# Kernel optimization log

Hardware: AMD Instinct MI355X
Metric: run time of the kernel (lower is better)

Reference implementation:

```python
import jax, jax.numpy as jnp
import numpy as np

# NOTE: SoftAttn (not shown in source) is assumed to be a channel-wise softmax over the
# kernel_size**2 attention maps, as is standard in involution/dynamic-conv designs.

def conv2d(x, w, b=None, stride=1, pad=0, dil=1):
    y = jax.lax.conv_general_dilated(
        x, w, (stride, stride), [(pad, pad), (pad, pad)],
        rhs_dilation=(dil, dil), dimension_numbers=('NCHW', 'OIHW', 'NCHW'))
    return y if b is None else y + b[None, :, None, None]

def prelu(x, a):
    return jnp.where(x >= 0, x, a * x)

def pixel_shuffle(x, r):
    b, c, h, w = x.shape
    x = x.reshape(b, c // (r * r), r, r, h, w)
    x = x.transpose(0, 1, 4, 2, 5, 3)  # b, c', h, r, w, r
    return x.reshape(b, c // (r * r), h * r, w * r)

def aflb(x, aw, ab, fw):
    # Adaptive Fine-grained Local Block: per-position attention over k^2 taps,
    # broadcast across input channels, then contracted with the conv weight.
    k = 3
    C = x.shape[1]
    att = jax.nn.softmax(conv2d(x, aw, ab, pad=1), axis=1)  # [b, k*k, H, W]
    # unfold (channel-major, spatial-minor, matching torch F.unfold)
    p = jax.lax.conv_general_dilated_patches(
        x, (k, k), (1, 1), [(1, 1), (1, 1)],
        dimension_numbers=('NCHW', 'OIHW', 'NCHW'))  # [b, C*k*k, H, W]
    b_, _, H, W = p.shape
    p = p.reshape(b_, C, k * k, H, W)
    atx = p * att[:, None]  # broadcast attention over channels
    return jnp.einsum('bcphw,ocp->bohw', atx, fw.reshape(fw.shape[0], C, k * k))

def rmrs(x, wa, ba, wb, bb, wc, bc, awA, abA, fwA, awB, abB, fwB):
    o = jnp.concatenate([
        conv2d(x, wa, ba, pad=1),
        conv2d(x, wb, bb, pad=2, dil=2),
        conv2d(x, wc, bc, pad=3, dil=3)], axis=1)
    o = aflb(o, awA, abA, fwA)
    o = aflb(o, awB, abB, fwB)
    return jax.nn.relu(o + x)


def setup_inputs() -> dict:
    key = jax.random.key(0)
    ks = iter(jax.random.split(key, 64))
    def rn(shape, s=0.05):
        return jax.random.normal(next(ks), shape, jnp.float32) * s
    a = lambda: jnp.full((1,), 0.25, jnp.float32)
    d = dict(
        ms_up=rn((2, 4, 256, 256), 1.0),
        ms_org=rn((2, 4, 64, 64), 1.0),
        pan=rn((2, 1, 256, 256), 1.0),
        w_up4=rn((64, 4, 3, 3)), b_up4=jnp.zeros(64, jnp.float32), a_up4=a(),
        w_blk53=rn((30, 5, 3, 3)), b_blk53=jnp.zeros(30, jnp.float32), a_blk53=a(),
        w_blk43=rn((30, 4, 3, 3)), b_blk43=jnp.zeros(30, jnp.float32), a_blk43=a(),
        w1a=rn((20, 60, 3, 3)), b1a=jnp.zeros(20, jnp.float32),
        w1b=rn((20, 60, 3, 3)), b1b=jnp.zeros(20, jnp.float32),
        w1c=rn((20, 60, 3, 3)), b1c=jnp.zeros(20, jnp.float32),
        aw1=rn((9, 60, 3, 3)), ab1=jnp.zeros(9, jnp.float32), fw1=rn((60, 60, 3, 3)),
        aw2=rn((9, 60, 3, 3)), ab2=jnp.zeros(9, jnp.float32), fw2=rn((60, 60, 3, 3)),
        w_blk2=rn((30, 60, 3, 3)), b_blk2=jnp.zeros(30, jnp.float32), a_blk2=a(),
        w2a=rn((10, 30, 3, 3)), b2a=jnp.zeros(10, jnp.float32),
        w2b=rn((10, 30, 3, 3)), b2b=jnp.zeros(10, jnp.float32),
        w2c=rn((10, 30, 3, 3)), b2c=jnp.zeros(10, jnp.float32),
        aw3=rn((9, 30, 3, 3)), ab3=jnp.zeros(9, jnp.float32), fw3=rn((30, 30, 3, 3)),
        aw4=rn((9, 30, 3, 3)), ab4=jnp.zeros(9, jnp.float32), fw4=rn((30, 30, 3, 3)),
        w_c6=rn((4, 30, 3, 3)), b_c6=jnp.zeros(4, jnp.float32),
    )
    return d


def reference(ms_up, ms_org, pan,
              w_up4, b_up4, a_up4,
              w_blk53, b_blk53, a_blk53,
              w_blk43, b_blk43, a_blk43,
              w1a, b1a, w1b, b1b, w1c, b1c,
              aw1, ab1, fw1, aw2, ab2, fw2,
              w_blk2, b_blk2, a_blk2,
              w2a, b2a, w2b, b2b, w2c, b2c,
              aw3, ab3, fw3, aw4, ab4, fw4,
              w_c6, b_c6):
    ms_org_up = prelu(pixel_shuffle(conv2d(ms_org, w_up4, b_up4, pad=1), 4), a_up4)
    data1 = jnp.concatenate([ms_org_up, pan], axis=1)  # [b,5,H,W]
    pan_conv = prelu(conv2d(data1, w_blk53, b_blk53, pad=1), a_blk53)
    ms_up_conv = prelu(conv2d(ms_up, w_blk43, b_blk43, pad=1), a_blk43)
    out1 = jnp.concatenate([ms_up_conv, pan_conv], axis=1)  # [b,60,H,W]
    out2 = rmrs(out1, w1a, b1a, w1b, b1b, w1c, b1c, aw1, ab1, fw1, aw2, ab2, fw2)
    out3 = prelu(conv2d(out2, w_blk2, b_blk2, pad=1), a_blk2)  # [b,30,H,W]
    out3 = rmrs(out3, w2a, b2a, w2b, b2b, w2c, b2c, aw3, ab3, fw3, aw4, ab4, fw4)
    out8 = conv2d(out3, w_c6, b_c6, pad=1)
    return out8 + ms_up
```

## Files before the change

kernel.cpp:

```cpp
#include <hip/hip_runtime.h>

typedef __attribute__((ext_vector_type(8))) short short8;
typedef __attribute__((ext_vector_type(4))) float f32x4;
typedef __attribute__((ext_vector_type(4))) int i32x4;

#define HW 65536

__device__ __forceinline__ float bf2f(unsigned short u){
    union { unsigned int i; float f; } x; x.i = ((unsigned int)u) << 16; return x.f;
}
__device__ __forceinline__ unsigned short f2bf(float f){
    union { float f; unsigned int i; } x; x.f = f;
    unsigned int r = x.i + 0x7fffu + ((x.i >> 16) & 1u);
    return (unsigned short)(r >> 16);
}
__device__ __forceinline__ unsigned int pack2(float a, float b){
    return (unsigned int)f2bf(a) | ((unsigned int)f2bf(b) << 16);
}
__device__ __forceinline__ i32x4 addrelu4(i32x4 a, i32x4 b){
    i32x4 o;
#pragma unroll
    for (int k = 0; k < 4; ++k) {
        unsigned int ua = (unsigned int)a[k], ub = (unsigned int)b[k];
        float x0 = bf2f((unsigned short)(ua & 0xffff)) + bf2f((unsigned short)(ub & 0xffff));
        float x1 = bf2f((unsigned short)(ua >> 16))    + bf2f((unsigned short)(ub >> 16));
        o[k] = (int)(((unsigned int)f2bf(fmaxf(x0, 0.f))) |
                     ((unsigned int)f2bf(fmaxf(x1, 0.f)) << 16));
    }
    return o;
}

template<int PRELU>
__global__ __launch_bounds__(256, 4) void sconv2_k(
    const unsigned short* __restrict__ inA, const unsigned short* __restrict__ wfA,
    const float* __restrict__ biasA, const float* __restrict__ alA, int coffA,
    const unsigned short* __restrict__ inB, const unsigned short* __restrict__ wfB,
    const float* __restrict__ biasB, const float* __restrict__ alB, int coffB,
    unsigned short* __restrict__ outb, int cpad)
{
    constexpr int KK = 1;
    constexpr int CPIN = 32, SGR = 4, SGRP = 5, SPX = 66;
    constexpr int NSTGDW = 3 * SPX * SGRP * 4;
    constexpr int ODP = 20;
    constexpr int OUTOFF = NSTGDW;
    __shared__ __align__(16) unsigned int sm[NSTGDW + 64 * ODP];
    const int tid = threadIdx.x;
    const int lane = tid & 63, wv = tid >> 6;
    const int col = lane & 15, g = lane >> 4;
    const int bx = blockIdx.x;
    const int xcd = bx & 7, t = bx >> 3;
    const int y0 = xcd * 32 + (t & 31);
    const int x0 = ((t >> 5) & 3) * 64;
    const int which = blockIdx.z >> 1, b = blockIdx.z & 1;
    const unsigned short* in = which ? inB : inA;
    const unsigned short* wfrag = which ? wfB : wfA;
    const float* bias = which ? biasB : biasA;
    const float* alphap = which ? alB : alA;
    const int coff = which ? coffB : coffA;
    const unsigned short* inb = in + (size_t)b * HW * CPIN;

#pragma unroll
    for (int rr = 0; rr < 3; ++rr) {
        const int yy = y0 + rr - 1;
        for (int u = tid; u < SPX * SGR; u += 256) {
            const int slot = u & (SGR - 1), px = u / SGR;
            const int xx = x0 - 1 + px;
            i32x4 v = {0,0,0,0};
            if ((unsigned)yy < 256u && (unsigned)xx < 256u)
                v = *(const i32x4*)(inb + (size_t)(yy * 256 + xx) * CPIN + slot * 8);
            *(i32x4*)&sm[((rr * SPX + px) * SGRP + slot) * 4] = v;
        }
    }
    if (tid < 64) sm[OUTOFF + tid * ODP + 15] = 0;
    __syncthreads();

    const short8* wp = (const short8*)wfrag;
    f32x4 acc[2][2];
#pragma unroll
    for (int mt = 0; mt < 2; ++mt)
#pragma unroll
        for (int c = 0; c < 2; ++c) acc[mt][c] = (f32x4){0.f,0.f,0.f,0.f};
#pragma unroll
    for (int tap = 0; tap < 9; ++tap) {
        const int dy = tap / 3 - 1, dx = tap % 3 - 1;
        const int rl = dy + 1;
        short8 af[2];
#pragma unroll
        for (int mt = 0; mt < 2; ++mt)
            af[mt] = wp[(tap * 2 + mt) * 64 + lane];
        const int pl = 1 + wv * 16 + col + dx;
        const int c2 = tap & 1;
        short8 bf = *(const short8*)&sm[((rl * SPX + pl) * SGRP + g) * 4];
#pragma unroll
        for (int mt = 0; mt < 2; ++mt)
            acc[mt][c2] = __builtin_amdgcn_mfma_f32_16x16x32_bf16(af[mt], bf, acc[mt][c2], 0, 0, 0);
    }
    const float al = PRELU ? __ldg(alphap) : 0.f;
    const int px = wv * 16 + col;
#pragma unroll
    for (int mt = 0; mt < 2; ++mt) {
        const f32x4 a = acc[mt][0] + acc[mt][1];
#pragma unroll
        for (int e = 0; e < 2; ++e) {
            const int rb = mt * 16 + g * 4 + e * 2;
            if (rb < 30) {
                float v0 = a[e * 2]     + __ldg(bias + rb);
                float v1 = a[e * 2 + 1] + ((rb + 1 < 30) ? __ldg(bias + rb + 1) : 0.f);
                if (PRELU) { v0 = v0 >= 0.f ? v0 : al * v0; v1 = v1 >= 0.f ? v1 : al * v1; }
                if (rb + 1 >= 30) v1 = 0.f;
                sm[OUTOFF + px * ODP + (rb >> 1)] = pack2(v0, v1);
            }
        }
    }
    __syncthreads();
    {
        const int slot = tid & 3, opx = tid >> 2;
        i32x4 v = *(i32x4*)&sm[OUTOFF + opx * ODP + slot * 4];
        const size_t go = ((size_t)b * HW + (size_t)y0 * 256 + x0 + opx) * cpad + coff + slot * 8;
        *(i32x4*)(outb + go) = v;
    }
}

template<int KK, int PRELU>
__global__ __launch_bounds__(256, 4) void sconv_k(
    const unsigned short* __restrict__ in,
    const unsigned short* __restrict__ wfrag,
    const float* __restrict__ bias,
    const float* __restrict__ alphap,
    unsigned short* __restrict__ outb, int cpad, int coff)
{
    constexpr int CPIN = KK * 32, SGR = KK * 4, SGRP = SGR + 1, SPX = 66;
    constexpr int NSTGDW = 3 * SPX * SGRP * 4;
    constexpr int ODP = 20;
    constexpr int OUTOFF = NSTGDW;
    __shared__ __align__(16) unsigned int sm[NSTGDW + 64 * ODP];
    const int tid = threadIdx.x;
    const int lane = tid & 63, wv = tid >> 6;
    const int col = lane & 15, g = lane >> 4;
    const int bx = blockIdx.x;
    const int xcd = bx & 7, t = bx >> 3;
    const int y0 = xcd * 32 + (t & 31);
    const int x0 = ((t >> 5) & 3) * 64;
    const int b = blockIdx.z;
    const unsigned short* inb = in + (size_t)b * HW * CPIN;

#pragma unroll
    for (int rr = 0; rr < 3; ++rr) {
        const int yy = y0 + rr - 1;
        for (int u = tid; u < SPX * SGR; u += 256) {
            const int slot = u & (SGR - 1), px = u / SGR;
            const int xx = x0 - 1 + px;
            i32x4 v = {0,0,0,0};
            if ((unsigned)yy < 256u && (unsigned)xx < 256u)
                v = *(const i32x4*)(inb + (size_t)(yy * 256 + xx) * CPIN + slot * 8);
            *(i32x4*)&sm[((rr * SPX + px) * SGRP + slot) * 4] = v;
        }
    }
    if (tid < 64) sm[OUTOFF + tid * ODP + 15] = 0;
    __syncthreads();

    const short8* wp = (const short8*)wfrag;
    f32x4 acc[2][2];
#pragma unroll
    for (int mt = 0; mt < 2; ++mt)
#pragma unroll
        for (int c = 0; c < 2; ++c) acc[mt][c] = (f32x4){0.f,0.f,0.f,0.f};
#pragma unroll
    for (int tap = 0; tap < 9; ++tap) {
        const int dy = tap / 3 - 1, dx = tap % 3 - 1;
        const int rl = dy + 1;
        short8 af[2][KK];
#pragma unroll
        for (int mt = 0; mt < 2; ++mt)
#pragma unroll
            for (int kk = 0; kk < KK; ++kk)
                af[mt][kk] = wp[((tap * 2 + mt) * KK + kk) * 64 + lane];
        const int pl = 1 + wv * 16 + col + dx;
#pragma unroll
        for (int kk = 0; kk < KK; ++kk) {
            const int c2 = (KK == 2) ? kk : (tap & 1);
            short8 bf = *(const short8*)&sm[((rl * SPX + pl) * SGRP + kk * 4 + g) * 4];
#pragma unroll
            for (int mt = 0; mt < 2; ++mt)
                acc[mt][c2] = __builtin_amdgcn_mfma_f32_16x16x32_bf16(af[mt][kk], bf, acc[mt][c2], 0, 0, 0);
        }
    }
    const float al = PRELU ? __ldg(alphap) : 0.f;
    const int px = wv * 16 + col;
#pragma unroll
    for (int mt = 0; mt < 2; ++mt) {
        const f32x4 a = acc[mt][0] + acc[mt][1];
#pragma unroll
        for (int e = 0; e < 2; ++e) {
            const int rb = mt * 16 + g * 4 + e * 2;
            if (rb < 30) {
                float v0 = a[e * 2]     + __ldg(bias + rb);
                float v1 = a[e * 2 + 1] + ((rb + 1 < 30) ? __ldg(bias + rb + 1) : 0.f);
                if (PRELU) { v0 = v0 >= 0.f ? v0 : al * v0; v1 = v1 >= 0.f ? v1 : al * v1; }
                if (rb + 1 >= 30) v1 = 0.f;
                sm[OUTOFF + px * ODP + (rb >> 1)] = pack2(v0, v1);
            }
        }
    }
    __syncthreads();
    {
        const int slot = tid & 3, opx = tid >> 2;
        i32x4 v = *(i32x4*)&sm[OUTOFF + opx * ODP + slot * 4];
        const size_t go = ((size_t)b * HW + (size_t)y0 * 256 + x0 + opx) * cpad + coff + slot * 8;
        *(i32x4*)(outb + go) = v;
    }
}

template<int KK, int MR>
__global__ __launch_bounds__(256, 4) void trident_s(
    const unsigned short* __restrict__ in,
    const unsigned short* __restrict__ wf0, const unsigned short* __restrict__ wf1,
    const unsigned short* __restrict__ wf2,
    const float* __restrict__ b0, const float* __restrict__ b1, const float* __restrict__ b2,
    unsigned short* __restrict__ outb)
{
    constexpr int CPIN = KK * 32, CPAD = KK * 32;
    constexpr int SGR = KK * 4, SGRP = SGR + 1, SPX = 70;
    constexpr int MT_ = (KK == 2) ? 2 : 1;
    constexpr int CPP = KK * 4, ODP = (CPP + 1) * 4;
    constexpr int NSTGDW = 3 * SPX * SGRP * 4;
    constexpr int OUTOFF = NSTGDW;
    constexpr int NG1 = SPX * SGR;
    constexpr int NIT2 = (2 * NG1 + 255) / 256;
    __shared__ __align__(16) unsigned int sm[NSTGDW + 64 * ODP];
    const int tid = threadIdx.x;
    const int lane = tid & 63, wv = tid >> 6;
    const int col = lane & 15, g = lane >> 4;
    const int bx = blockIdx.x;
    const int xcd = bx & 7, t = bx >> 3;
    const int y0 = xcd * 32 + (t & 31);
    const int x0 = ((t >> 5) & 3) * 64;
    const int b = blockIdx.z;
    const unsigned short* inb = in + (size_t)b * HW * CPIN;

    auto stage_row = [&](int srow, int yy) {
        for (int u = tid; u < NG1; u += 256) {
            const int slot = u & (SGR - 1), px = u / SGR;
            const int xx = x0 - 3 + px;
            i32x4 v = {0,0,0,0};
            if ((unsigned)yy < 256u && (unsigned)xx < 256u)
                v = *(const i32x4*)(inb + (size_t)(yy * 256 + xx) * CPIN + slot * 8);
            *(i32x4*)&sm[((srow * SPX + px) * SGRP + slot) * 4] = v;
        }
    };
    i32x4 Rp[NIT2], Rq[NIT2];
    auto issue_into = [&](int d, i32x4* R) {
#pragma unroll
        for (int it = 0; it < NIT2; ++it) {
            const int u = tid + it * 256;
            i32x4 v = {0,0,0,0};
            if (u < 2 * NG1) {
                const int r = (u >= NG1) ? 1 : 0;
                const int uu = u - r * NG1;
                const int slot = uu & (SGR - 1), px = uu / SGR;
                const int yy = y0 + (r ? d : -d);
                const int xx = x0 - 3 + px;
                if ((unsigned)yy < 256u && (unsigned)xx < 256u)
                    v = *(const i32x4*)(inb + (size_t)(yy * 256 + xx) * CPIN + slot * 8);
            }
            R[it] = v;
        }
    };
    auto write_from = [&](i32x4* R) {
#pragma unroll
        for (int it = 0; it < NIT2; ++it) {
            const int u = tid + it * 256;
            if (u < 2 * NG1) {
                const int r = (u >= NG1) ? 1 : 0;
                const int uu = u - r * NG1;
                const int slot = uu & (SGR - 1), px = uu / SGR;
                *(i32x4*)&sm[(((1 + r) * SPX + px) * SGRP + slot) * 4] = R[it];
            }
        }
    };
    auto do_conv = [&](int d, const unsigned short* wfx, const float* bs, int which) {
        const short8* wp = (const short8*)wfx;
        f32x4 acc[MT_][2];
#pragma unroll
        for (int mt = 0; mt < MT_; ++mt)
#pragma unroll
            for (int c = 0; c < 2; ++c) acc[mt][c] = (f32x4){0.f,0.f,0.f,0.f};
#pragma unroll
        for (int tap = 0; tap < 9; ++tap) {
            const int dy = tap / 3 - 1, dx = tap % 3 - 1;
            const int rl = (dy == 0) ? 0 : (dy < 0 ? 1 : 2);
            short8 af[MT_][KK];
#pragma unroll
            for (int mt = 0; mt < MT_; ++mt)
#pragma unroll
                for (int kk = 0; kk < KK; ++kk)
                    af[mt][kk] = wp[((tap * MT_ + mt) * KK + kk) * 64 + lane];
            const int pl = 3 + wv * 16 + col + dx * d;
#pragma unroll
            for (int kk = 0; kk < KK; ++kk) {
                const int c2 = (KK == 2) ? kk : (tap & 1);
                short8 bf = *(const short8*)&sm[((rl * SPX + pl) * SGRP + kk * 4 + g) * 4];
#pragma unroll
                for (int mt = 0; mt < MT_; ++mt)
                    acc[mt][c2] = __builtin_amdgcn_mfma_f32_16x16x32_bf16(af[mt][kk], bf, acc[mt][c2], 0, 0, 0);
            }
        }
        const int px = wv * 16 + col;
#pragma unroll
        for (int mt = 0; mt < MT_; ++mt) {
            const f32x4 a = acc[mt][0] + acc[mt][1];
#pragma unroll
            for (int e = 0; e < 2; ++e) {
                const int rb = mt * 16 + g * 4 + e * 2;
                if (rb < MR) {
                    float v0 = a[e * 2]     + __ldg(bs + rb);
                    float v1 = a[e * 2 + 1] + ((rb + 1 < MR) ? __ldg(bs + rb + 1) : 0.f);
                    if (rb + 1 >= MR) v1 = 0.f;
                    sm[OUTOFF + px * ODP + ((which * MR + rb) >> 1)] = pack2(v0, v1);
                }
            }
        }
    };

    stage_row(0, y0); stage_row(1, y0 - 1); stage_row(2, y0 + 1);
    issue_into(2, Rp);
    issue_into(3, Rq);
    if (tid < 64) {
#pragma unroll
        for (int dwp = 3 * MR / 2; dwp < CPP * 4; ++dwp) sm[OUTOFF + tid * ODP + dwp] = 0;
    }
    __syncthreads();

    do_conv(1, wf0, b0, 0);
    __syncthreads();
    write_from(Rp);
    __syncthreads();

    do_conv(2, wf1, b1, 1);
    __syncthreads();
    write_from(Rq);
    __syncthreads();

    do_conv(3, wf2, b2, 2);
    __syncthreads();

    for (int u = tid; u < 64 * CPP; u += 256) {
        const int slot = u & (CPP - 1), opx = u / CPP;
        i32x4 v = *(i32x4*)&sm[OUTOFF + opx * ODP + slot * 4];
        const size_t go = ((size_t)b * HW + (size_t)y0 * 256 + x0 + opx) * CPAD + slot * 8;
        *(i32x4*)(outb + go) = v;
    }
}

template<int KK, int RPB, int RES>
__global__ __launch_bounds__(256, 4) void aflb_p(
    const unsigned short* __restrict__ in,
    const unsigned short* __restrict__ awf, const float* __restrict__ ab,
    const unsigned short* __restrict__ fwf,
    const unsigned short* __restrict__ res,
    unsigned short* __restrict__ outb)
{
    constexpr int CPIN = KK * 32, MTT = 2 * KK, CPAD = 16 * MTT;
    constexpr int SROWS = RPB + 2, SPX = 66, SGR = KK * 4, SGRP = SGR + 1;
    constexpr int CPP = CPAD / 8, ODP = (CPP + 1) * 4;
    constexpr int NSTGDW = SROWS * SPX * SGRP * 4;
    constexpr int ATOFF = NSTGDW;
    constexpr int NATT = RPB * 64 * 9;
    constexpr int OUTOFF = ATOFF + NATT;
    __shared__ __align__(16) unsigned int sm[OUTOFF + RPB * 64 * ODP];

    const int tid = threadIdx.x;
    const int lane = tid & 63, wv = tid >> 6;
    const int col = lane & 15, g = lane >> 4;
    const int bx = blockIdx.x;
    const int xcd = bx & 7, t = bx >> 3;
    const int y0 = (RPB == 1) ? (xcd * 32 + (t & 31)) : (xcd * 32 + (t & 15) * 2);
    const int xseg = (RPB == 1) ? ((t >> 5) & 3) : ((t >> 4) & 3);
    const int x0 = xseg * 64;
    const int b = blockIdx.z;
    const unsigned short* inb = in + (size_t)b * HW * CPIN;

    for (int u = tid; u < SROWS * SPX * SGR; u += 256) {
        const int slot = u & (SGR - 1);
        const int px = (u / SGR) % SPX;
        const int row = u / (SGR * SPX);
        const int yy = y0 + row - 1, xx = x0 - 1 + px;
        i32x4 v = {0,0,0,0};
        if ((unsigned)yy < 256u && (unsigned)xx < 256u)
            v = *(const i32x4*)(inb + (size_t)(yy * 256 + xx) * CPIN + slot * 8);
        *(i32x4*)&sm[((row * SPX + px) * SGRP + slot) * 4] = v;
    }
    __syncthreads();

    const short8* awp = (const short8*)awf;
    const short8* fwp = (const short8*)fwf;

    constexpr int NF1 = (RPB == 1) ? 1 : 2;
    const int arow = (RPB == 1) ? 0 : (wv >> 1);
    const int apx0 = (RPB == 1) ? (wv * 16) : ((wv & 1) * 32);
    f32x4 aacc[NF1][2];
#pragma unroll
    for (int nf = 0; nf < NF1; ++nf)
#pragma unroll
        for (int c = 0; c < 2; ++c) aacc[nf][c] = (f32x4){0.f,0.f,0.f,0.f};
#pragma unroll
    for (int tap = 0; tap < 9; ++tap) {
        const int dy = tap / 3 - 1, dx = tap % 3 - 1;
        const int rl = arow + dy + 1;
        short8 afa[KK];
#pragma unroll
        for (int kk = 0; kk < KK; ++kk)
            afa[kk] = awp[(tap * KK + kk) * 64 + lane];
#pragma unroll
        for (int nf = 0; nf < NF1; ++nf) {
            const int pl = 1 + apx0 + nf * 16 + col + dx;
#pragma unroll
            for (int kk = 0; kk < KK; ++kk) {
                const int c2 = (KK == 2) ? kk : (tap & 1);
                short8 bf = *(const short8*)&sm[((rl * SPX + pl) * SGRP + kk * 4 + g) * 4];
                aacc[nf][c2] = __builtin_amdgcn_mfma_f32_16x16x32_bf16(afa[kk], bf, aacc[nf][c2], 0, 0, 0);
            }
        }
    }
#pragma unroll
    for (int nf = 0; nf < NF1; ++nf) {
        const f32x4 aa = aacc[nf][0] + aacc[nf][1];
        float v[4];
        float m = -1e30f;
#pragma unroll
        for (int r = 0; r < 4; ++r) {
            const int row = g * 4 + r;
            v[r] = (row < 9) ? (aa[r] + __ldg(ab + row)) : -1e30f;
            m = fmaxf(m, v[r]);
        }
        m = fmaxf(m, __shfl_xor(m, 16));
        m = fmaxf(m, __shfl_xor(m, 32));
        float e[4]; float s = 0.f;
#pragma unroll
        for (int r = 0; r < 4; ++r) { e[r] = (g * 4 + r < 9) ? __expf(v[r] - m) : 0.f; s += e[r]; }
        s += __shfl_xor(s, 16);
        s += __shfl_xor(s, 32);
        const float inv = 1.f / s;
        const int px = apx0 + nf * 16 + col;
#pragma unroll
        for (int r = 0; r < 4; ++r) {
            const int row = g * 4 + r;
            if (row < 9) sm[ATOFF + (arow * 64 + px) * 9 + row] = __float_as_uint(e[r] * inv);
        }
    }
    __syncthreads();

    const int prow = (RPB == 1) ? 0 : (wv >> 1);
    const int mth  = (RPB == 1) ? (wv >> 1) : 0;
    const int nfh  = wv & 1;
    f32x4 acc[2][2];
#pragma unroll
    for (int mtl = 0; mtl < 2; ++mtl)
#pragma unroll
        for (int nf = 0; nf < 2; ++nf) acc[mtl][nf] = (f32x4){0.f,0.f,0.f,0.f};
#pragma unroll
    for (int tap = 0; tap < 9; ++tap) {
        const int dy = tap / 3 - 1, dx = tap % 3 - 1;
        const int rl = prow + dy + 1;
        float av[2];
#pragma unroll
        for (int nf = 0; nf < 2; ++nf)
            av[nf] = __uint_as_float(sm[ATOFF + (prow * 64 + nfh * 32 + nf * 16 + col) * 9 + tap]);
        short8 af[2][KK];
#pragma unroll
        for (int mtl = 0; mtl < 2; ++mtl)
#pragma unroll
            for (int kk = 0; kk < KK; ++kk)
                af[mtl][kk] = fwp[((tap * MTT + (RPB == 1 ? mth * 2 + mtl : mtl)) * KK + kk) * 64 + lane];
#pragma unroll
        for (int nf = 0; nf < 2; ++nf) {
            const int pl = 1 + nfh * 32 + nf * 16 + col + dx;
            f32x4 p[2];
            p[0] = (f32x4){0.f,0.f,0.f,0.f}; p[1] = (f32x4){0.f,0.f,0.f,0.f};
#pragma unroll
            for (int kk = 0; kk < KK; ++kk) {
                short8 bf = *(const short8*)&sm[((rl * SPX + pl) * SGRP + kk * 4 + g) * 4];
#pragma unroll
                for (int mtl = 0; mtl < 2; ++mtl)
                    p[mtl] = __builtin_amdgcn_mfma_f32_16x16x32_bf16(af[mtl][kk], bf, p[mtl], 0, 0, 0);
            }
#pragma unroll
            for (int mtl = 0; mtl < 2; ++mtl)
#pragma unroll
                for (int r = 0; r < 4; ++r)
                    acc[mtl][nf][r] = fmaf(av[nf], p[mtl][r], acc[mtl][nf][r]);
        }
    }
    __syncthreads();

#pragma unroll
    for (int mtl = 0; mtl < 2; ++mtl) {
        const int mt = (RPB == 1) ? (mth * 2 + mtl) : mtl;
#pragma unroll
        for (int nf = 0; nf < 2; ++nf) {
            const int px = nfh * 32 + nf * 16 + col;
            const int base = OUTOFF + ((RPB == 2 ? prow * 64 : 0) + px) * ODP;
            const int rp = mt * 8 + g * 2;
            unsigned long long w =
                (unsigned long long)pack2(acc[mtl][nf][0], acc[mtl][nf][1]) |
                ((unsigned long long)pack2(acc[mtl][nf][2], acc[mtl][nf][3]) << 32);
            *(unsigned long long*)&sm[base + rp] = w;
        }
    }
    __syncthreads();

    constexpr int NOUT = RPB * 64 * CPP;
    for (int u = tid; u < NOUT; u += 256) {
        const int slot = u & (CPP - 1);
        const int px = (u / CPP) & 63;
        const int r = (RPB == 2) ? (u / (CPP * 64)) : 0;
        i32x4 v = *(i32x4*)&sm[OUTOFF + ((r * 64 + px) * ODP) + slot * 4];
        const size_t go = ((size_t)b * HW + (size_t)(y0 + r) * 256 + x0 + px) * CPAD + slot * 8;
        if (RES) v = addrelu4(v, *(const i32x4*)(res + go));
        *(i32x4*)(outb + go) = v;
    }
}

__global__ __launch_bounds__(256, 4) void final_k(
    const unsigned short* __restrict__ in,
    const unsigned short* __restrict__ wfrag,
    const float* __restrict__ bias,
    const float* __restrict__ msup, float* __restrict__ outf)
{
    constexpr int CPIN = 32, NF = 2;
    const int lane = threadIdx.x & 63, wv = threadIdx.x >> 6;
    const int col = lane & 15, g = lane >> 4;
    const int bx = blockIdx.x;
    const int xcd = bx & 7, t = bx >> 3;
    const int y = xcd * 32 + (t & 31);
    const int xh = t >> 5;
    const int b = blockIdx.z;
    const int x0 = xh * 128 + wv * 32;

    const unsigned short* inb = in + (size_t)b * HW * CPIN;
    const short8 kz = {0,0,0,0,0,0,0,0};
    const short8* wp = (const short8*)wfrag;

    f32x4 acc[NF];
#pragma unroll
    for (int nf = 0; nf < NF; ++nf) acc[nf] = (f32x4){0.f,0.f,0.f,0.f};
#pragma unroll
    for (int tap = 0; tap < 9; ++tap) {
        const int dy = tap / 3 - 1, dx = tap % 3 - 1;
        const int yy = y + dy;
        const bool yok = (unsigned)yy < 256u;
        const short8 af = wp[tap * 64 + lane];
#pragma unroll
        for (int nf = 0; nf < NF; ++nf) {
            const int xx = x0 + nf * 16 + col + dx;
            const bool ok = yok && ((unsigned)xx < 256u);
            const int pix = ok ? (yy * 256 + xx) : 0;
            short8 bf = *(const short8*)(inb + (size_t)pix * CPIN + g * 8);
            if (!ok) bf = kz;
            acc[nf] = __builtin_amdgcn_mfma_f32_16x16x32_bf16(af, bf, acc[nf], 0, 0, 0);
        }
    }
#pragma unroll
    for (int nf = 0; nf < NF; ++nf) {
        const int pix = y * 256 + x0 + nf * 16 + col;
        if (g == 0) {
#pragma unroll
            for (int r = 0; r < 4; ++r) {
                const size_t oi = ((size_t)b * 4 + r) * HW + pix;
                outf[oi] = acc[nf][r] + __ldg(bias + r) + msup[oi];
            }
        }
    }
}

struct PrepDesc { const float* src; int cout, cin, kksh, mtsh, flags, dstoff, n; };
struct PrepArgs { PrepDesc d[18]; };

__global__ __launch_bounds__(256) void prep_k(PrepArgs pa, unsigned short* __restrict__ wb)
{
    const PrepDesc d = pa.d[blockIdx.y];
    const int e = blockIdx.x * 256 + threadIdx.x;
    if (e >= d.n) return;
    const int j = e & 7;
    const int lane = (e >> 3) & 63;
    const int i512 = e >> 9;
    const int kk = i512 & ((1 << d.kksh) - 1);
    const int mt = (i512 >> d.kksh) & ((1 << d.mtsh) - 1);
    const int tap = i512 >> (d.kksh + d.mtsh);
    const int rpos = mt * 16 + (lane & 15);
    const int kpos = kk * 32 + (lane >> 4) * 8 + j;
    int o = rpos, ic = kpos;
    bool ok = true;
    if (d.flags & 2) {
        if (rpos < 30) o = rpos;
        else if (rpos >= 32 && rpos < 62) o = rpos - 2;
        else ok = false;
    }
    if (d.flags & 1) {
        if (kpos < 30) ic = kpos;
        else if (kpos >= 32 && kpos < 62) ic = kpos - 2;
        else ok = false;
    }
    float v = 0.f;
    if (ok && o < d.cout && ic < d.cin) v = d.src[(o * d.cin + ic) * 9 + tap];
    wb[d.dstoff + e] = f2bf(v);
}

template<int CIN, int COUT, int OCB, int H, int W>
__launch_bounds__(256)
__global__ void upconv_k(const float* __restrict__ in, const float* __restrict__ wgt,
                         const float* __restrict__ bias, float* __restrict__ out)
{
    constexpr int HWp = H * W;
    constexpr int NOCB = COUT / OCB;
    const int tx = threadIdx.x;
    const int lx = tx & 63, ly = tx >> 6;
    const int gx = blockIdx.x * 64 + lx;
    const int gy = blockIdx.y * 4 + ly;
    const int b = blockIdx.z / NOCB;
    const int ocb = blockIdx.z % NOCB;
    const int pixp = gy * W + gx;
    const float* inb = in + (size_t)b * CIN * HWp;

    int off[9]; float mul[9];
#pragma unroll
    for (int dy = 0; dy < 3; ++dy)
#pragma unroll
        for (int dx = 0; dx < 3; ++dx) {
            int p = dy * 3 + dx;
            int yy = gy + dy - 1, xx = gx + dx - 1;
            bool okp = ((unsigned)yy < (unsigned)H) && ((unsigned)xx < (unsigned)W);
            off[p] = okp ? (yy * W + xx) : 0;
            mul[p] = okp ? 1.f : 0.f;
        }
    float acc[OCB];
#pragma unroll
    for (int o = 0; o < OCB; ++o) acc[o] = 0.f;
    const float* wbase = wgt + (size_t)(ocb * OCB) * CIN * 9;
#pragma unroll
    for (int ic = 0; ic < CIN; ++ic) {
        const float* ip = inb + (size_t)ic * HWp;
        float tv[9];
#pragma unroll
        for (int p = 0; p < 9; ++p) tv[p] = __ldg(ip + off[p]) * mul[p];
#pragma unroll
        for (int o = 0; o < OCB; ++o) {
            const float* wq = wbase + (size_t)(o * CIN + ic) * 9;
#pragma unroll
            for (int p = 0; p < 9; ++p) acc[o] = fmaf(tv[p], wq[p], acc[o]);
        }
    }
#pragma unroll
    for (int o = 0; o < OCB; ++o)
        out[((size_t)b * COUT + ocb * OCB + o) * HWp + pixp] = acc[o] + __ldg(bias + ocb * OCB + o);
}

__global__ __launch_bounds__(256) void build_inputs(
    const float* __restrict__ tup, const float* __restrict__ pan,
    const float* __restrict__ aup, const float* __restrict__ msup,
    unsigned short* __restrict__ data1, unsigned short* __restrict__ msb)
{
    const int i = blockIdx.x * 256 + threadIdx.x;
    const int b = i >> 16, pixp = i & 65535;
    const int y = pixp >> 8, x = pixp & 255;
    unsigned short o[32];
#pragma unroll
    for (int c = 0; c < 32; ++c) o[c] = 0;
    unsigned short* dst;
    if (blockIdx.y == 0) {
        const float a = __ldg(aup);
#pragma unroll
        for (int c = 0; c < 4; ++c) {
            const int ch = c * 16 + (y & 3) * 4 + (x & 3);
            float v = tup[(((size_t)b * 64 + ch) << 12) + ((y >> 2) << 6) + (x >> 2)];
            v = (v >= 0.f) ? v : a * v;
            o[c] = f2bf(v);
        }
        o[4] = f2bf(pan[((size_t)b << 16) + pixp]);
        dst = data1;
    } else {
#pragma unroll
        for (int c = 0; c < 4; ++c)
            o[c] = f2bf(msup[(((size_t)b * 4 + c) << 16) + pixp]);
        dst = msb;
    }
    short8* dp = (short8*)(dst + (size_t)i * 32);
#pragma unroll
    for (int q = 0; q < 4; ++q) {
        short8 s;
#pragma unroll
        for (int r = 0; r < 8; ++r) s[r] = (short)o[q * 8 + r];
        dp[q] = s;
    }
}

extern "C" void kernel_launch(void* const* d_in, const int* in_sizes, int n_in,
                              void* d_out, int out_size, void* d_ws, size_t ws_size,
                              hipStream_t stream) {
    const float* ms_up  = (const float*)d_in[0];
    const float* ms_org = (const float*)d_in[1];
    const float* pan    = (const float*)d_in[2];
    const float* w_up4  = (const float*)d_in[3];
    const float* b_up4  = (const float*)d_in[4];
    const float* a_up4  = (const float*)d_in[5];
    const float* w_blk53= (const float*)d_in[6];
    const float* b_blk53= (const float*)d_in[7];
    const float* a_blk53= (const float*)d_in[8];
    const float* w_blk43= (const float*)d_in[9];
    const float* b_blk43= (const float*)d_in[10];
    const float* a_blk43= (const float*)d_in[11];
    const float* w1a=(const float*)d_in[12]; const float* b1a=(const float*)d_in[13];
    const float* w1b=(const float*)d_in[14]; const float* b1b=(const float*)d_in[15];
    const float* w1c=(const float*)d_in[16]; const float* b1c=(const float*)d_in[17];
    const float* aw1=(const float*)d_in[18]; const float* ab1=(const float*)d_in[19];
    const float* fw1=(const float*)d_in[20];
    const float* aw2=(const float*)d_in[21]; const float* ab2=(const float*)d_in[22];
    const float* fw2=(const float*)d_in[23];
    const float* w_blk2=(const float*)d_in[24]; const float* b_blk2=(const float*)d_in[25]; const float* a_blk2=(const float*)d_in[26];
    const float* w2a=(const float*)d_in[27]; const float* b2a=(const float*)d_in[28];
    const float* w2b=(const float*)d_in[29]; const float* b2b=(const float*)d_in[30];
    const float* w2c=(const float*)d_in[31]; const float* b2c=(const float*)d_in[32];
    const float* aw3=(const float*)d_in[33]; const float* ab3=(const float*)d_in[34];
    const float* fw3=(const float*)d_in[35];
    const float* aw4=(const float*)d_in[36]; const float* ab4=(const float*)d_in[37];
    const float* fw4=(const float*)d_in[38];
    const float* w_c6=(const float*)d_in[39]; const float* b_c6=(const float*)d_in[40];

    float* out = (float*)d_out;
    char* ws = (char*)d_ws;

    const size_t BIG = (size_t)2 * HW * 64 * 2;
    const size_t HALF = BIG / 2;
    unsigned short* bufA = (unsigned short*)(ws);
    unsigned short* bufB = (unsigned short*)(ws + BIG);
    unsigned short* bufC = (unsigned short*)(ws + 2 * BIG);
    unsigned short* data1 = bufC;
    float*          t_up  = (float*)(ws + 2 * BIG + HALF);
    unsigned short* msb   = bufB;
    unsigned short* bufD = bufC;
    unsigned short* bufE = bufB;
    unsigned short* bufF = bufA;
    unsigned short* wb = (unsigned short*)(ws + 3 * BIG);

    if (ws_size < 3 * BIG + 1000000) return;

    PrepArgs pa;
    int off = 0, li = 0;
    auto add = [&](const float* s, int cout, int cin, int mtsh, int kksh, int flags) {
        const int n = 9 << (mtsh + kksh + 9);
        pa.d[li].src = s; pa.d[li].cout = cout; pa.d[li].cin = cin;
        pa.d[li].kksh = kksh; pa.d[li].mtsh = mtsh; pa.d[li].flags = flags;
        pa.d[li].dstoff = off; pa.d[li].n = n;
        int ret = off; off += n; ++li; return ret;
    };
    const int o_blk43 = add(w_blk43, 30, 4, 1, 0, 0);
    const int o_blk53 = add(w_blk53, 30, 5, 1, 0, 0);
    const int o_w1a   = add(w1a, 20, 60, 1, 1, 1);
    const int o_w1b   = add(w1b, 20, 60, 1, 1, 1);
    const int o_w1c   = add(w1c, 20, 60, 1, 1, 1);
    const int o_aw1   = add(aw1,  9, 60, 0, 1, 0);
    const int o_fw1   = add(fw1, 60, 60, 2, 1, 0);
    const int o_aw2   = add(aw2,  9, 60, 0, 1, 0);
    const int o_fw2   = add(fw2, 60, 60, 2, 1, 2);
    const int o_blk2  = add(w_blk2, 30, 60, 1, 1, 1);
    const int o_w2a   = add(w2a, 10, 30, 0, 0, 0);
    const int o_w2b   = add(w2b, 10, 30, 0, 0, 0);
    const int o_w2c   = add(w2c, 10, 30, 0, 0, 0);
    const int o_aw3   = add(aw3,  9, 30, 0, 0, 0);
    const int o_fw3   = add(fw3, 30, 30, 1, 0, 0);
    const int o_aw4   = add(aw4,  9, 30, 0, 0, 0);
    const int o_fw4   = add(fw4, 30, 30, 1, 0, 0);
    const int o_c6    = add(w_c6,  4, 30, 0, 0, 0);

    prep_k<<<dim3(144, 18), 256, 0, stream>>>(pa, wb);

    upconv_k<4, 64, 16, 64, 64><<<dim3(1, 16, 8), 256, 0, stream>>>(ms_org, w_up4, b_up4, t_up);
    build_inputs<<<dim3(512, 2), 256, 0, stream>>>(t_up, pan, a_up4, ms_up, data1, msb);

    const dim3 B256(256);
    const dim3 G1(1024, 1, 2);
    const dim3 G2(1024, 1, 4);
    const dim3 GH(512, 1, 2);

    sconv2_k<1><<<G2,B256,0,stream>>>(msb, wb+o_blk43, b_blk43, a_blk43, 0,
                                      data1, wb+o_blk53, b_blk53, a_blk53, 32,
                                      bufA, 64);

    trident_s<2,20><<<G1,B256,0,stream>>>(bufA, wb+o_w1a, wb+o_w1b, wb+o_w1c, b1a, b1b, b1c, bufB);
    aflb_p<2,1,0><<<G1,B256,0,stream>>>(bufB, wb+o_aw1, ab1, wb+o_fw1, nullptr, bufC);
    aflb_p<2,1,1><<<G1,B256,0,stream>>>(bufC, wb+o_aw2, ab2, wb+o_fw2, bufA,   bufB);

    sconv_k<2,1><<<G1,B256,0,stream>>>(bufB, wb+o_blk2, b_blk2, a_blk2, bufD, 32, 0);

    trident_s<1,10><<<G1,B256,0,stream>>>(bufD, wb+o_w2a, wb+o_w2b, wb+o_w2c, b2a, b2b, b2c, bufE);
    aflb_p<1,2,0><<<GH,B256,0,stream>>>(bufE, wb+o_aw3, ab3, wb+o_fw3, nullptr, bufF);
    aflb_p<1,2,1><<<GH,B256,0,stream>>>(bufF, wb+o_aw4, ab4, wb+o_fw4, bufD,   bufE);

    final_k<<<GH,B256,0,stream>>>(bufE, wb+o_c6, b_c6, ms_up, out);
}
```

Before: 201.1 us.

## Run trident dilations concurrently across wavefronts on 2x32 tiles

Replaces the sequential three-pass trident conv (one dilation at a time, with restaging and barriers between passes) by a 384-thread block. Each of six wavefronts handles one dilation for one of two output rows over a 32-pixel tile. An 8-row halo is staged once, which removes the intermediate barriers and register-held prefetches. The cost is a larger halo overhead per output pixel and changed occupancy from the new launch bounds.

```diff
diff --git a/kernel.cpp b/kernel.cpp
--- a/kernel.cpp
+++ b/kernel.cpp
@@ -38,7 +38,6 @@
     const float* __restrict__ biasB, const float* __restrict__ alB, int coffB,
     unsigned short* __restrict__ outb, int cpad)
 {
-    constexpr int KK = 1;
     constexpr int CPIN = 32, SGR = 4, SGRP = 5, SPX = 66;
     constexpr int NSTGDW = 3 * SPX * SGRP * 4;
     constexpr int ODP = 20;
@@ -212,7 +211,7 @@
 }
 
 template<int KK, int MR>
-__global__ __launch_bounds__(256, 4) void trident_s(
+__global__ __launch_bounds__(384, (KK == 2 ? 5 : 8)) void trident_p(
     const unsigned short* __restrict__ in,
     const unsigned short* __restrict__ wf0, const unsigned short* __restrict__ wf1,
     const unsigned short* __restrict__ wf2,
@@ -220,134 +219,105 @@
     unsigned short* __restrict__ outb)
 {
     constexpr int CPIN = KK * 32, CPAD = KK * 32;
-    constexpr int SGR = KK * 4, SGRP = SGR + 1, SPX = 70;
+    constexpr int SGR = KK * 4, SGRP = SGR + 1, SPX = 38, SROWS = 8;
     constexpr int MT_ = (KK == 2) ? 2 : 1;
     constexpr int CPP = KK * 4, ODP = (CPP + 1) * 4;
-    constexpr int NSTGDW = 3 * SPX * SGRP * 4;
-    constexpr int OUTOFF = NSTGDW;
-    constexpr int NG1 = SPX * SGR;
-    constexpr int NIT2 = (2 * NG1 + 255) / 256;
-    __shared__ __align__(16) unsigned int sm[NSTGDW + 64 * ODP];
+    constexpr int NSTGDW = SROWS * SPX * SGRP * 4;
+    __shared__ __align__(16) unsigned int sm[NSTGDW];
+
     const int tid = threadIdx.x;
     const int lane = tid & 63, wv = tid >> 6;
     const int col = lane & 15, g = lane >> 4;
     const int bx = blockIdx.x;
     const int xcd = bx & 7, t = bx >> 3;
-    const int y0 = xcd * 32 + (t & 31);
-    const int x0 = ((t >> 5) & 3) * 64;
+    const int y0 = xcd * 32 + (t & 15) * 2;
+    const int x0 = ((t >> 4) & 7) * 32;
     const int b = blockIdx.z;
     const unsigned short* inb = in + (size_t)b * HW * CPIN;
 
-    auto stage_row = [&](int srow, int yy) {
-        for (int u = tid; u < NG1; u += 256) {
-            const int slot = u & (SGR - 1), px = u / SGR;
-            const int xx = x0 - 3 + px;
-            i32x4 v = {0,0,0,0};
-            if ((unsigned)yy < 256u && (unsigned)xx < 256u)
-                v = *(const i32x4*)(inb + (size_t)(yy * 256 + xx) * CPIN + slot * 8);
-            *(i32x4*)&sm[((srow * SPX + px) * SGRP + slot) * 4] = v;
-        }
-    };
-    i32x4 Rp[NIT2], Rq[NIT2];
-    auto issue_into = [&](int d, i32x4* R) {
-#pragma unroll
-        for (int it = 0; it < NIT2; ++it) {
-            const int u = tid + it * 256;
-            i32x4 v = {0,0,0,0};
-            if (u < 2 * NG1) {
-                const int r = (u >= NG1) ? 1 : 0;
-                const int uu = u - r * NG1;
-                const int slot = uu & (SGR - 1), px = uu / SGR;
-                const int yy = y0 + (r ? d : -d);
-                const int xx = x0 - 3 + px;
-                if ((unsigned)yy < 256u && (unsigned)xx < 256u)
-                    v = *(const i32x4*)(inb + (size_t)(yy * 256 + xx) * CPIN + slot * 8);
-            }
-            R[it] = v;
-        }
-    };
-    auto write_from = [&](i32x4* R) {
-#pragma unroll
-        for (int it = 0; it < NIT2; ++it) {
-            const int u = tid + it * 256;
-            if (u < 2 * NG1) {
-                const int r = (u >= NG1) ? 1 : 0;
-                const int uu = u - r * NG1;
-                const int slot = uu & (SGR - 1), px = uu / SGR;
-                *(i32x4*)&sm[(((1 + r) * SPX + px) * SGRP + slot) * 4] = R[it];
-            }
-        }
-    };
-    auto do_conv = [&](int d, const unsigned short* wfx, const float* bs, int which) {
-        const short8* wp = (const short8*)wfx;
-        f32x4 acc[MT_][2];
+    for (int u = tid; u < SROWS * SPX * SGR; u += 384) {
+        const int slot = u & (SGR - 1);
+        const int px = (u / SGR) % SPX;
+        const int row = u / (SGR * SPX);
+        const int yy = y0 + row - 3, xx = x0 - 3 + px;
+        i32x4 v = {0,0,0,0};
+        if ((unsigned)yy < 256u && (unsigned)xx < 256u)
+            v = *(const i32x4*)(inb + (size_t)(yy * 256 + xx) * CPIN + slot * 8);
+        *(i32x4*)&sm[((row * SPX + px) * SGRP + slot) * 4] = v;
+    }
+    __syncthreads();
+
+    const int r = (wv >= 3) ? 1 : 0;
+    const int dil = wv - r * 3, d = dil + 1;
+    const unsigned short* wfx = (dil == 0) ? wf0 : ((dil == 1) ? wf1 : wf2);
+    const float* bs = (dil == 0) ? b0 : ((dil == 1) ? b1 : b2);
+    const short8* wp = (const short8*)wfx;
+
+    f32x4 acc[MT_][2][2];
+#pragma unroll
+    for (int mt = 0; mt < MT_; ++mt)
+#pragma unroll
+        for (int nf = 0; nf < 2; ++nf)
+#pragma unroll
+            for (int c = 0; c < 2; ++c) acc[mt][nf][c] = (f32x4){0.f,0.f,0.f,0.f};
+
+#pragma unroll
+    for (int tap = 0; tap < 9; ++tap) {
+        const int dy = tap / 3 - 1, dx = tap % 3 - 1;
+        const int rl = 3 + r + dy * d;
+        short8 af[MT_][KK];
 #pragma unroll
         for (int mt = 0; mt < MT_; ++mt)
 #pragma unroll
-            for (int c = 0; c < 2; ++c) acc[mt][c] = (f32x4){0.f,0.f,0.f,0.f};
-#pragma unroll
-        for (int tap = 0; tap < 9; ++tap) {
-            const int dy = tap / 3 - 1, dx = tap % 3 - 1;
-            const int rl = (dy == 0) ? 0 : (dy < 0 ? 1 : 2);
-            short8 af[MT_][KK];
-#pragma unroll
-            for (int mt = 0; mt < MT_; ++mt)
-#pragma unroll
-                for (int kk = 0; kk < KK; ++kk)
-                    af[mt][kk] = wp[((tap * MT_ + mt) * KK + kk) * 64 + lane];
-            const int pl = 3 + wv * 16 + col + dx * d;
+            for (int kk = 0; kk < KK; ++kk)
+                af[mt][kk] = wp[((tap * MT_ + mt) * KK + kk) * 64 + lane];
+#pragma unroll
+        for (int nf = 0; nf < 2; ++nf) {
+            const int pl = 3 + nf * 16 + col + dx * d;
 #pragma unroll
             for (int kk = 0; kk < KK; ++kk) {
                 const int c2 = (KK == 2) ? kk : (tap & 1);
                 short8 bf = *(const short8*)&sm[((rl * SPX + pl) * SGRP + kk * 4 + g) * 4];
 #pragma unroll
                 for (int mt = 0; mt < MT_; ++mt)
-                    acc[mt][c2] = __builtin_amdgcn_mfma_f32_16x16x32_bf16(af[mt][kk], bf, acc[mt][c2], 0, 0, 0);
+                    acc[mt][nf][c2] = __builtin_amdgcn_mfma_f32_16x16x32_bf16(af[mt][kk], bf, acc[mt][nf][c2], 0, 0, 0);
             }
         }
-        const int px = wv * 16 + col;
+    }
+    __syncthreads();
+
+#pragma unroll
+    for (int nf = 0; nf < 2; ++nf) {
+        const int px = nf * 16 + col;
+        const int base = (r * 32 + px) * ODP;
 #pragma unroll
         for (int mt = 0; mt < MT_; ++mt) {
-            const f32x4 a = acc[mt][0] + acc[mt][1];
+            const f32x4 a = acc[mt][nf][0] + acc[mt][nf][1];
 #pragma unroll
             for (int e = 0; e < 2; ++e) {
                 const int rb = mt * 16 + g * 4 + e * 2;
                 if (rb < MR) {
-                    float v0 = a[e * 2]     + __ldg(bs + rb);
-                    float v1 = a[e * 2 + 1] + ((rb + 1 < MR) ? __ldg(bs + rb + 1) : 0.f);
-                    if (rb + 1 >= MR) v1 = 0.f;
-                    sm[OUTOFF + px * ODP + ((which * MR + rb) >> 1)] = pack2(v0, v1);
+                    float v0 = a[e * 2] + __ldg(bs + rb);
+                    float v1 = (rb + 1 < MR) ? a[e * 2 + 1] + __ldg(bs + rb + 1) : 0.f;
+                    sm[base + ((dil * MR + rb) >> 1)] = pack2(v0, v1);
                 }
             }
         }
-    };
-
-    stage_row(0, y0); stage_row(1, y0 - 1); stage_row(2, y0 + 1);
-    issue_into(2, Rp);
-    issue_into(3, Rq);
-    if (tid < 64) {
-#pragma unroll
-        for (int dwp = 3 * MR / 2; dwp < CPP * 4; ++dwp) sm[OUTOFF + tid * ODP + dwp] = 0;
-    }
-    __syncthreads();
-
-    do_conv(1, wf0, b0, 0);
-    __syncthreads();
-    write_from(Rp);
-    __syncthreads();
-
-    do_conv(2, wf1, b1, 1);
-    __syncthreads();
-    write_from(Rq);
-    __syncthreads();
-
-    do_conv(3, wf2, b2, 2);
-    __syncthreads();
-
-    for (int u = tid; u < 64 * CPP; u += 256) {
-        const int slot = u & (CPP - 1), opx = u / CPP;
-        i32x4 v = *(i32x4*)&sm[OUTOFF + opx * ODP + slot * 4];
-        const size_t go = ((size_t)b * HW + (size_t)y0 * 256 + x0 + opx) * CPAD + slot * 8;
+    }
+    {
+        constexpr int NPAD = CPP * 4 - 3 * MR / 2;
+        if (tid < 64 * NPAD) {
+            const int pxr = tid / NPAD, dwp = 3 * MR / 2 + tid % NPAD;
+            sm[pxr * ODP + dwp] = 0;
+        }
+    }
+    __syncthreads();
+
+    for (int u = tid; u < 64 * CPP; u += 384) {
+        const int slot = u & (CPP - 1), pxr = u / CPP;
+        const int rr = pxr >> 5, opx = pxr & 31;
+        i32x4 v = *(i32x4*)&sm[pxr * ODP + slot * 4];
+        const size_t go = ((size_t)b * HW + (size_t)(y0 + rr) * 256 + x0 + opx) * CPAD + slot * 8;
         *(i32x4*)(outb + go) = v;
     }
 }
@@ -777,22 +747,23 @@
     upconv_k<4, 64, 16, 64, 64><<<dim3(1, 16, 8), 256, 0, stream>>>(ms_org, w_up4, b_up4, t_up);
     build_inputs<<<dim3(512, 2), 256, 0, stream>>>(t_up, pan, a_up4, ms_up, data1, msb);
 
-    const dim3 B256(256);
+    const dim3 B256(256), B384(384);
     const dim3 G1(1024, 1, 2);
     const dim3 G2(1024, 1, 4);
+    const dim3 GP(1024, 1, 2);
     const dim3 GH(512, 1, 2);
 
     sconv2_k<1><<<G2,B256,0,stream>>>(msb, wb+o_blk43, b_blk43, a_blk43, 0,
                                       data1, wb+o_blk53, b_blk53, a_blk53, 32,
                                       bufA, 64);
 
-    trident_s<2,20><<<G1,B256,0,stream>>>(bufA, wb+o_w1a, wb+o_w1b, wb+o_w1c, b1a, b1b, b1c, bufB);
+    trident_p<2,20><<<GP,B384,0,stream>>>(bufA, wb+o_w1a, wb+o_w1b, wb+o_w1c, b1a, b1b, b1c, bufB);
     aflb_p<2,1,0><<<G1,B256,0,stream>>>(bufB, wb+o_aw1, ab1, wb+o_fw1, nullptr, bufC);
     aflb_p<2,1,1><<<G1,B256,0,stream>>>(bufC, wb+o_aw2, ab2, wb+o_fw2, bufA,   bufB);
 
     sconv_k<2,1><<<G1,B256,0,stream>>>(bufB, wb+o_blk2, b_blk2, a_blk2, bufD, 32, 0);
 
-    trident_s<1,10><<<G1,B256,0,stream>>>(bufD, wb+o_w2a, wb+o_w2b, wb+o_w2c, b2a, b2b, b2c, bufE);
+    trident_p<1,10><<<GP,B384,0,stream>>>(bufD, wb+o_w2a, wb+o_w2b, wb+o_w2c, b2a, b2b, b2c, bufE);
     aflb_p<1,2,0><<<GH,B256,0,stream>>>(bufE, wb+o_aw3, ab3, wb+o_fw3, nullptr, bufF);
     aflb_p<1,2,1><<<GH,B256,0,stream>>>(bufF, wb+o_aw4, ab4, wb+o_fw4, bufD,   bufE);
 
```

Measured after the change: 190.1 us. 5.5% less time.
